# Kernel optimization log

Hardware: AMD Instinct MI355X
Metric: run time of the kernel (lower is better)

The kernel has to match this reference:

```python
import jax, jax.numpy as jnp
import numpy as np

N_U = 100000   # num users
N_V = 50000    # num items
K = 5          # num_support (rating levels)
E_SUP = 400000 # edges per support
E = 500000     # decoder prediction edges
D_IN = 512     # input_dim
D_GCN = 500    # gcn_hidden_dim (D_GCN % K == 0)
D_SIDE = 128   # side_feat_dim
H_SIDE = 64    # side_hidden_dim
D_ENC = 128    # encode_hidden_dim
NB = 3         # num_basis
NC = 5         # num_classes


def setup_inputs() -> dict:
    key = jax.random.key(0)
    ks = jax.random.split(key, 20)
    s = 0.05
    return {
        # sparse supports (COO): user_supports[i] = (N_U,N_V), item_supports[i] = transpose
        "sup_user_idx": jax.random.randint(ks[0], (K, E_SUP), 0, N_U),
        "sup_item_idx": jax.random.randint(ks[1], (K, E_SUP), 0, N_V),
        "sup_vals": jax.random.uniform(ks[2], (K, E_SUP), dtype=jnp.float32),
        "user_inputs": jax.random.normal(ks[3], (N_U, D_IN), dtype=jnp.float32),
        "item_inputs": jax.random.normal(ks[4], (N_V, D_IN), dtype=jnp.float32),
        "user_side_inputs": jax.random.normal(ks[5], (N_U, D_SIDE), dtype=jnp.float32),
        "item_side_inputs": jax.random.normal(ks[6], (N_V, D_SIDE), dtype=jnp.float32),
        "user_edge_idx": jax.random.randint(ks[7], (E,), 0, N_U),
        "item_edge_idx": jax.random.randint(ks[8], (E,), 0, N_V),
        # parameters
        "W_enc": jax.random.normal(ks[9], (K, D_IN, D_GCN // K), dtype=jnp.float32) * s,
        "Wu1": jax.random.normal(ks[10], (D_SIDE, H_SIDE), dtype=jnp.float32) * s,
        "bu1": jnp.zeros((H_SIDE,), dtype=jnp.float32),
        "Wi1": jax.random.normal(ks[11], (D_SIDE, H_SIDE), dtype=jnp.float32) * s,
        "bi1": jnp.zeros((H_SIDE,), dtype=jnp.float32),
        "Wu2": jax.random.normal(ks[12], (D_GCN + H_SIDE, D_ENC), dtype=jnp.float32) * s,
        "Wi2": jax.random.normal(ks[13], (D_GCN + H_SIDE, D_ENC), dtype=jnp.float32) * s,
        "dec_W": jax.random.normal(ks[14], (NB, D_ENC, D_ENC), dtype=jnp.float32) * s,
        "dec_cls": jax.random.normal(ks[15], (NB, NC), dtype=jnp.float32) * s,
    }


def _forward(sup_user_idx, sup_item_idx, sup_vals, user_inputs, item_inputs,
             user_side_inputs, item_side_inputs, user_edge_idx, item_edge_idx,
             W_enc, Wu1, bu1, Wi1, bi1, Wu2, Wi2, dec_W, dec_cls):
    # ---- StackGCNEncoder ----
    tmp_u = jnp.einsum("nd,kdf->knf", user_inputs, W_enc)  # [K, N_U, D_GCN//K]
    tmp_v = jnp.einsum("nd,kdf->knf", item_inputs, W_enc)  # [K, N_V, D_GCN//K]

    def agg_user(rows, cols, vals, xv):  # sparse.mm(user_support, tmp_v)
        return jax.ops.segment_sum(vals[:, None] * xv[cols], rows, num_segments=N_U)

    def agg_item(rows, cols, vals, xu):  # sparse.mm(item_support, tmp_u)
        return jax.ops.segment_sum(vals[:, None] * xu[rows], cols, num_segments=N_V)

    user_hidden = jax.vmap(agg_user)(sup_user_idx, sup_item_idx, sup_vals, tmp_v)  # [K,N_U,f]
    item_hidden = jax.vmap(agg_item)(sup_user_idx, sup_item_idx, sup_vals, tmp_u)  # [K,N_V,f]
    # concat over supports along feature dim
    user_gcn = jax.nn.relu(jnp.transpose(user_hidden, (1, 0, 2)).reshape(N_U, D_GCN))
    item_gcn = jax.nn.relu(jnp.transpose(item_hidden, (1, 0, 2)).reshape(N_V, D_GCN))

    # ---- dense1 (relu, bias) ----
    user_side = jax.nn.relu(user_side_inputs @ Wu1 + bu1)
    item_side = jax.nn.relu(item_side_inputs @ Wi1 + bi1)

    # ---- concat + dense2 (identity activation, no bias) ----
    user_embed = jnp.concatenate([user_gcn, user_side], axis=1) @ Wu2  # [N_U, D_ENC]
    item_embed = jnp.concatenate([item_gcn, item_side], axis=1) @ Wi2  # [N_V, D_ENC]

    # ---- Decoder (bilinear basis, identity activation) ----
    u = user_embed[user_edge_idx]  # [E, D_ENC]
    v = item_embed[item_edge_idx]  # [E, D_ENC]
    basis = jnp.stack([jnp.sum((u @ dec_W[b]) * v, axis=1) for b in range(NB)], axis=1)  # [E, NB]
    return basis @ dec_cls  # [E, NC]


def reference(sup_user_idx, sup_item_idx, sup_vals, user_inputs, item_inputs,
              user_side_inputs, item_side_inputs, user_edge_idx, item_edge_idx,
              W_enc, Wu1, bu1, Wi1, bi1, Wu2, Wi2, dec_W, dec_cls):
    return _forward(sup_user_idx, sup_item_idx, sup_vals, user_inputs, item_inputs,
                    user_side_inputs, item_side_inputs, user_edge_idx, item_edge_idx,
                    W_enc, Wu1, bu1, Wi1, bi1, Wu2, Wi2, dec_W, dec_cls)
```

## Files before the change

### kernel.cpp

```cpp
#include <hip/hip_runtime.h>

#define NU 100000
#define NV 50000
#define KSUP 5
#define ESUP 400000
#define NEDGE (KSUP * ESUP)
#define NE 500000
#define DIN 512
#define DGCN 500
#define FSUP 100
#define DSIDE 128
#define HSIDE 64
#define DENC 128
#define NBAS 3
#define NCLS 5

#define TMPW 640
#define XW 576

#define BNODE 512
#define RU 196
#define RV 98
#define NBU (KSUP * RU)
#define NBV (KSUP * RV)
#define NBT (NBU + NBV)
#define CAPU 2560
#define CAPV 5120
#define CHUNK 8192

#define GU128 782
#define GV128 391
#define GU64 1563
#define GV64 782
#define GBIN 245
#define PB1 (GBIN + 1280)
#define PB2 (PB1 + 288)
#define PB3 (PB2 + 288)
#define PB4 (PB3 + 48)
#define PTOT (PB4 + 75000)

__device__ __forceinline__ ushort f2bf(float x) {
    union { float f; unsigned u; } c; c.f = x;
    unsigned r = (c.u + 0x7FFFu + ((c.u >> 16) & 1u)) >> 16;
    return (ushort)r;
}
__device__ __forceinline__ float lof(uint g) { return __uint_as_float(g << 16); }
__device__ __forceinline__ float hif(uint g) { return __uint_as_float(g & 0xffff0000u); }

typedef __attribute__((ext_vector_type(4))) float f32x4;
typedef __attribute__((ext_vector_type(8))) short bf16x8;
typedef __attribute__((address_space(3))) void lds_void;
typedef const __attribute__((address_space(1))) void glob_void;
typedef unsigned long long ull;

__device__ __forceinline__ void gemm_body(
    const ushort* __restrict__ A, const ushort* __restrict__ BT,
    ushort* __restrict__ Cout, int M, int N, int K, int ldc,
    int rowBase, int colBase)
{
    __shared__ ushort As[128 * 64];
    __shared__ ushort Bs[128 * 64];
    const int t = threadIdx.x;
    const int lane = t & 63;
    const int w = t >> 6;
    const int wr = w >> 1, wc = w & 1;

    f32x4 acc[4][4] = {};

    for (int k0 = 0; k0 < K; k0 += 64) {
        #pragma unroll
        for (int i = 0; i < 4; ++i) {
            int chi = i * 256 + t;
            int r = chi >> 3;
            int c = (((chi >> 3) & 7) ^ (chi & 7)) * 8;
            int ga = rowBase + r; if (ga > M - 1) ga = M - 1;
            __builtin_amdgcn_global_load_lds(
                (glob_void*)(A + (size_t)ga * K + k0 + c),
                (lds_void*)(As + (size_t)chi * 8), 16, 0, 0);
            int gb = colBase + r; if (gb > N - 1) gb = N - 1;
            __builtin_amdgcn_global_load_lds(
                (glob_void*)(BT + (size_t)gb * K + k0 + c),
                (lds_void*)(Bs + (size_t)chi * 8), 16, 0, 0);
        }
        __syncthreads();

        #pragma unroll
        for (int kk = 0; kk < 2; ++kk) {
            bf16x8 af[4], bfr[4];
            const int cb2 = (kk * 32 + (lane >> 4) * 8) * 2;
            #pragma unroll
            for (int mi = 0; mi < 4; ++mi) {
                int r = wr * 64 + mi * 16 + (lane & 15);
                int off = (r * 128 + cb2) ^ ((r & 7) << 4);
                af[mi] = *(const bf16x8*)((const char*)As + off);
            }
            #pragma unroll
            for (int nj = 0; nj < 4; ++nj) {
                int r = wc * 64 + nj * 16 + (lane & 15);
                int off = (r * 128 + cb2) ^ ((r & 7) << 4);
                bfr[nj] = *(const bf16x8*)((const char*)Bs + off);
            }
            #pragma unroll
            for (int mi = 0; mi < 4; ++mi)
                #pragma unroll
                for (int nj = 0; nj < 4; ++nj)
                    acc[mi][nj] = __builtin_amdgcn_mfma_f32_16x16x32_bf16(
                        af[mi], bfr[nj], acc[mi][nj], 0, 0, 0);
        }
        __syncthreads();
    }

    #pragma unroll
    for (int mi = 0; mi < 4; ++mi) {
        #pragma unroll
        for (int q = 0; q < 4; ++q) {
            int gr = rowBase + wr * 64 + mi * 16 + (lane >> 4) * 4 + q;
            if (gr >= M) continue;
            #pragma unroll
            for (int nj = 0; nj < 4; ++nj) {
                int gc = colBase + wc * 64 + nj * 16 + (lane & 15);
                Cout[(size_t)gr * ldc + gc] = f2bf(acc[mi][nj][q]);
            }
        }
    }
}

__global__ __launch_bounds__(256) void gemm_bf16_k(
    const ushort* __restrict__ A, const ushort* __restrict__ BT,
    ushort* __restrict__ Cout, int M, int N, int K, int ldc)
{
    gemm_body(A, BT, Cout, M, N, K, ldc, blockIdx.y * 128, blockIdx.x * 128);
}

__global__ __launch_bounds__(256) void gemm_enc_k(
    const ushort* __restrict__ u_bf, const ushort* __restrict__ v_bf,
    const ushort* __restrict__ WencT2,
    ushort* __restrict__ tmpU, ushort* __restrict__ tmpV)
{
    int y = blockIdx.y;
    const ushort* A; ushort* C; int M, rowBase;
    if (y < GU128) { A = u_bf; C = tmpU; M = NU; rowBase = y * 128; }
    else           { A = v_bf; C = tmpV; M = NV; rowBase = (y - GU128) * 128; }
    gemm_body(A, WencT2, C, M, TMPW, 512, TMPW, rowBase, blockIdx.x * 128);
}

__global__ __launch_bounds__(256) void gemm_d2_k(
    const ushort* __restrict__ Xu, const ushort* __restrict__ Xv,
    const ushort* __restrict__ W2u, const ushort* __restrict__ W2i,
    ushort* __restrict__ embU, ushort* __restrict__ embV)
{
    int y = blockIdx.y;
    const ushort* A; const ushort* BT; ushort* C; int M, rowBase;
    if (y < GU128) { A = Xu; BT = W2u; C = embU; M = NU; rowBase = y * 128; }
    else           { A = Xv; BT = W2i; C = embV; M = NV; rowBase = (y - GU128) * 128; }
    gemm_body(A, BT, C, M, DENC, XW, DENC, rowBase, 0);
}

#define BM 64
#define BK 16
__global__ __launch_bounds__(256) void side_k(
    const float* __restrict__ uS, const float* __restrict__ vS,
    const float* __restrict__ Wu1, const float* __restrict__ bu1,
    const float* __restrict__ Wi1, const float* __restrict__ bi1,
    ushort* __restrict__ Xu, ushort* __restrict__ Xv)
{
    __shared__ float As[BK][BM + 4];
    __shared__ float Bs[BK][BM + 4];
    int b = blockIdx.x;
    const float *A, *B, *bias; ushort* X; int M, rowBase;
    if (b < GU64) { A = uS; B = Wu1; bias = bu1; X = Xu; M = NU; rowBase = b * 64; }
    else          { A = vS; B = Wi1; bias = bi1; X = Xv; M = NV; rowBase = (b - GU64) * 64; }
    const int K = DSIDE;
    const int t = threadIdx.x;
    const int ty = t >> 4, tx = t & 15;
    float acc[4][4] = {};

    for (int k0 = 0; k0 < K; k0 += BK) {
        #pragma unroll
        for (int p = 0; p < 4; ++p) {
            int r = p * 16 + (t >> 4), kk = t & 15;
            int gr = rowBase + r, gk = k0 + kk;
            As[kk][r] = (gr < M && gk < K) ? A[(size_t)gr * K + gk] : 0.f;
        }
        #pragma unroll
        for (int p = 0; p < 4; ++p) {
            int kk = p * 4 + (t >> 6), j = t & 63;
            int gk = k0 + kk;
            Bs[kk][j] = (j < HSIDE && gk < K) ? B[(size_t)gk * HSIDE + j] : 0.f;
        }
        __syncthreads();
        #pragma unroll
        for (int kk = 0; kk < BK; ++kk) {
            float4 a4 = *reinterpret_cast<const float4*>(&As[kk][ty * 4]);
            float4 b4 = *reinterpret_cast<const float4*>(&Bs[kk][tx * 4]);
            float aa[4] = {a4.x, a4.y, a4.z, a4.w};
            float bb[4] = {b4.x, b4.y, b4.z, b4.w};
            #pragma unroll
            for (int i = 0; i < 4; ++i)
                #pragma unroll
                for (int j = 0; j < 4; ++j)
                    acc[i][j] = fmaf(aa[i], bb[j], acc[i][j]);
        }
        __syncthreads();
    }
    #pragma unroll
    for (int i = 0; i < 4; ++i) {
        int gr = rowBase + ty * 4 + i;
        if (gr >= M) continue;
        #pragma unroll
        for (int j = 0; j < 4; ++j) {
            int gc = tx * 4 + j;
            if (gc < HSIDE)
                X[(size_t)gr * XW + 500 + gc] = f2bf(fmaxf(acc[i][j] + bias[gc], 0.f));
        }
    }
}

__global__ __launch_bounds__(256) void prep_k(
    const int* __restrict__ su, const int* __restrict__ si,
    const float* __restrict__ sv,
    int* __restrict__ bCnt, ull* __restrict__ bktU, ull* __restrict__ bktV,
    const float* __restrict__ W_enc, ushort* __restrict__ WencT2,
    const float* __restrict__ Wu2, const float* __restrict__ Wi2,
    ushort* __restrict__ W2ufT, ushort* __restrict__ W2ifT,
    const float* __restrict__ dec_W, ushort* __restrict__ decbf,
    const float* __restrict__ u_in, const float* __restrict__ v_in,
    ushort* __restrict__ u_bf, ushort* __restrict__ v_bf)
{
    __shared__ int lcnt[NBT];
    __shared__ int lbase[NBT];
    const int bid = blockIdx.x;
    const int t = threadIdx.x;

    if (bid < GBIN) {
        const int e0 = bid * CHUNK;
        for (int i = t; i < NBT; i += 256) lcnt[i] = 0;
        __syncthreads();
        for (int i = t; i < CHUNK; i += 256) {
            int e = e0 + i;
            if (e >= NEDGE) break;
            int k = e / ESUP;
            int r = su[e], c = si[e];
            atomicAdd(&lcnt[k * RU + (r >> 9)], 1);
            atomicAdd(&lcnt[NBU + k * RV + (c >> 9)], 1);
        }
        __syncthreads();
        for (int i = t; i < NBT; i += 256) {
            int n = lcnt[i];
            lbase[i] = n ? atomicAdd(&bCnt[i], n) : 0;
        }
        __syncthreads();
        for (int i = t; i < NBT; i += 256) lcnt[i] = 0;
        __syncthreads();
        for (int i = t; i < CHUNK; i += 256) {
            int e = e0 + i;
            if (e >= NEDGE) break;
            int k = e / ESUP;
            int r = su[e], c = si[e];
            ull vb = (ull)(unsigned)__float_as_int(sv[e]) << 32;
            int bu = k * RU + (r >> 9);
            int pu = lbase[bu] + atomicAdd(&lcnt[bu], 1);
            if (pu < CAPU)
                bktU[(size_t)bu * CAPU + pu] = vb | (uint)(((r & 511) << 16) | c);
            int bv = NBU + k * RV + (c >> 9);
            int pv = lbase[bv] + atomicAdd(&lcnt[bv], 1);
            if (pv < CAPV)
                bktV[(size_t)(bv - NBU) * CAPV + pv] = vb | (uint)(((c & 511) << 17) | r);
        }
    } else if (bid < PB1) {
        int idx = (bid - GBIN) * 256 + t;
        int np = idx >> 9, d = idx & 511;
        int k = np >> 7, f = np & 127;
        float v = (f < FSUP) ? W_enc[((size_t)k * DIN + d) * FSUP + f] : 0.f;
        WencT2[idx] = f2bf(v);
    } else if (bid < PB3) {
        int which = (bid < PB2) ? 0 : 1;
        int idx = (bid - (which ? PB2 : PB1)) * 256 + t;
        const float* W = which ? Wi2 : Wu2;
        ushort* out = which ? W2ifT : W2ufT;
        int j = idx / XW, c = idx - j * XW;
        float v = (c < DGCN + HSIDE) ? W[(size_t)c * DENC + j] : 0.f;
        out[idx] = f2bf(v);
    } else if (bid < PB4) {
        long i = ((long)(bid - PB3) * 256 + t) * 4;
        if (i < (long)NBAS * DENC * DENC) {
            float4 v = *(const float4*)(dec_W + i);
            ushort4 o;
            o.x = f2bf(v.x); o.y = f2bf(v.y); o.z = f2bf(v.z); o.w = f2bf(v.w);
            *(ushort4*)(decbf + i) = o;
        }
    } else {
        long i = ((long)(bid - PB4) * 256 + t) * 4;
        const long nu = (long)NU * 512;
        const float* src; ushort* dst;
        if (i < nu) { src = u_in; dst = u_bf; }
        else {
            i -= nu;
            if (i >= (long)NV * 512) return;
            src = v_in; dst = v_bf;
        }
        float4 v = *(const float4*)(src + i);
        ushort4 o;
        o.x = f2bf(v.x); o.y = f2bf(v.y); o.z = f2bf(v.z); o.w = f2bf(v.w);
        *(ushort4*)(dst + i) = o;
    }
}

__global__ __launch_bounds__(256) void scat3_k(
    const int* __restrict__ bCnt,
    const ull* __restrict__ bktU, const ull* __restrict__ bktV,
    int* __restrict__ rowPtrU, int* __restrict__ rowPtrV,
    ull* __restrict__ eU, ull* __restrict__ eV)
{
    __shared__ ull stage[CAPV];
    __shared__ int cnt[BNODE];
    __shared__ int rowOff[BNODE];
    __shared__ int part[256];
    __shared__ int bbl[NBT];
    const int t = threadIdx.x;
    const int b = blockIdx.x;
    const int isU = (b < NBU);

    {
        const int PER = (NBT + 255) / 256;
        int loc[6]; int ssum = 0;
        #pragma unroll
        for (int i = 0; i < PER; ++i) {
            int idx = t * PER + i;
            loc[i] = (idx < NBT) ? bCnt[idx] : 0;
            ssum += loc[i];
        }
        part[t] = ssum; __syncthreads();
        for (int off = 1; off < 256; off <<= 1) {
            int add = (t >= off) ? part[t - off] : 0;
            __syncthreads();
            part[t] += add;
            __syncthreads();
        }
        int bb = part[t] - ssum;
        int run = 0;
        #pragma unroll
        for (int i = 0; i < PER; ++i) {
            int idx = t * PER + i;
            if (idx < NBT) bbl[idx] = bb + run;
            run += loc[i];
        }
        __syncthreads();
    }
    if (b == 0 && t == 0) {
        rowPtrU[KSUP * NU] = NEDGE;
        rowPtrV[KSUP * NV] = NEDGE;
    }

    const ull* src;
    int n, k, baseN, base, NN;
    int* rp;
    if (isU) {
        k = b / RU; baseN = (b % RU) << 9;
        src = bktU + (size_t)b * CAPU;
        n = bCnt[b]; if (n > CAPU) n = CAPU;
        base = bbl[b]; NN = NU; rp = rowPtrU;
    } else {
        int bb2 = b - NBU;
        k = bb2 / RV; baseN = (bb2 % RV) << 9;
        src = bktV + (size_t)bb2 * CAPV;
        n = bCnt[b]; if (n > CAPV) n = CAPV;
        base = bbl[b] - NEDGE; NN = NV; rp = rowPtrV;
    }

    for (int i = t; i < BNODE; i += 256) cnt[i] = 0;
    __syncthreads();

    for (int i = t; i < n; i += 256) {
        ull en = __builtin_nontemporal_load(&src[i]);
        uint w0 = (uint)en;
        int local = isU ? (int)(w0 >> 16) : (int)(w0 >> 17);
        atomicAdd(&cnt[local], 1);
    }
    __syncthreads();

    int c0 = cnt[2 * t], c1 = cnt[2 * t + 1];
    int s = c0 + c1;
    part[t] = s;
    __syncthreads();
    for (int off = 1; off < 256; off <<= 1) {
        int add = (t >= off) ? part[t - off] : 0;
        __syncthreads();
        part[t] += add;
        __syncthreads();
    }
    int excl = part[t] - s;
    cnt[2 * t] = excl;          rowOff[2 * t] = excl;
    cnt[2 * t + 1] = excl + c0; rowOff[2 * t + 1] = excl + c0;
    __syncthreads();

    for (int i = t; i < BNODE; i += 256) {
        int node = baseN + i;
        if (node < NN) rp[k * NN + node] = base + rowOff[i];
    }

    for (int i = t; i < n; i += 256) {
        ull en = __builtin_nontemporal_load(&src[i]);
        uint w0 = (uint)en;
        int local; uint off4;
        if (isU) { local = (int)(w0 >> 16); off4 = (w0 & 0xFFFF) * (TMPW * 2); }
        else     { local = (int)(w0 >> 17); off4 = (w0 & 0x1FFFF) * (TMPW * 2); }
        int p = atomicAdd(&cnt[local], 1);
        stage[p] = (en & 0xFFFFFFFF00000000ull) | off4;
    }
    __syncthreads();

    ull* dst = (isU ? eU : eV) + base;
    for (int i = t; i < n; i += 256)
        __builtin_nontemporal_store(stage[i], &dst[i]);
}

template<int K0, int NK, int B, int NNODE>
__device__ __forceinline__ void agg_do(
    const int* __restrict__ rowPtr, const ull* __restrict__ eArr,
    const char* __restrict__ tSrc, int n, uint lane4,
    float* __restrict__ a0, float* __restrict__ a1)
{
    int s[NK], d[NK];
    #pragma unroll
    for (int kk = 0; kk < NK; ++kk) {
        int g = (K0 + kk) * NNODE + n;
        int ss = rowPtr[g];
        int ee = rowPtr[g + 1];
        s[kk] = ss; d[kk] = ee - ss;
    }
    uint ex[NK][B], ev[NK][B], gw[NK][B];
    #pragma unroll
    for (int kk = 0; kk < NK; ++kk)
        #pragma unroll
        for (int i = 0; i < B; ++i) {
            int idx = (i < d[kk]) ? i : 0;
            ull t = __builtin_nontemporal_load(&eArr[s[kk] + idx]);
            ex[kk][i] = (i < d[kk]) ? (uint)t : 0u;
            ev[kk][i] = (uint)(t >> 32);
        }
    #pragma unroll
    for (int kk = 0; kk < NK; ++kk)
        #pragma unroll
        for (int i = 0; i < B; ++i)
            gw[kk][i] = *(const uint*)(tSrc + (ex[kk][i] + lane4 + ((uint)(K0 + kk) << 8)));
    #pragma unroll
    for (int kk = 0; kk < NK; ++kk) {
        float x0 = 0.f, x1 = 0.f;
        #pragma unroll
        for (int i = 0; i < B; ++i)
            if (i < d[kk]) {
                float v = __uint_as_float(ev[kk][i]);
                x0 = fmaf(v, lof(gw[kk][i]), x0);
                x1 = fmaf(v, hif(gw[kk][i]), x1);
            }
        a0[K0 + kk] = x0; a1[K0 + kk] = x1;
    }
    #pragma unroll
    for (int kk = 0; kk < NK; ++kk) {
        if (d[kk] > B) {
            uint fx[B], fv[B], g1[B];
            #pragma unroll
            for (int i = 0; i < B; ++i) {
                int idx = (B + i < d[kk]) ? B + i : B;
                ull t = __builtin_nontemporal_load(&eArr[s[kk] + idx]);
                fx[i] = (B + i < d[kk]) ? (uint)t : 0u;
                fv[i] = (uint)(t >> 32);
            }
            #pragma unroll
            for (int i = 0; i < B; ++i)
                g1[i] = *(const uint*)(tSrc + (fx[i] + lane4 + ((uint)(K0 + kk) << 8)));
            #pragma unroll
            for (int i = 0; i < B; ++i)
                if (B + i < d[kk]) {
                    float v = __uint_as_float(fv[i]);
                    a0[K0 + kk] = fmaf(v, lof(g1[i]), a0[K0 + kk]);
                    a1[K0 + kk] = fmaf(v, hif(g1[i]), a1[K0 + kk]);
                }
            for (int p = 2 * B; p < d[kk]; ++p) {
                ull t = __builtin_nontemporal_load(&eArr[s[kk] + p]);
                uint g = *(const uint*)(tSrc + ((uint)t + lane4 + ((uint)(K0 + kk) << 8)));
                float v = __uint_as_float((uint)(t >> 32));
                a0[K0 + kk] = fmaf(v, lof(g), a0[K0 + kk]);
                a1[K0 + kk] = fmaf(v, hif(g), a1[K0 + kk]);
            }
        }
    }
}

__device__ __forceinline__ void agg_store(ushort* Xrow, int lane,
                                          const float* a0, const float* a1) {
    #pragma unroll
    for (int k = 0; k < KSUP; ++k) {
        uint payload = (uint)f2bf(fmaxf(a0[k], 0.f)) |
                       ((uint)f2bf(fmaxf(a1[k], 0.f)) << 16);
        if (lane < 50)
            __builtin_nontemporal_store(payload, (uint*)(Xrow + k * FSUP) + lane);
    }
    if (lane < 6)
        __builtin_nontemporal_store(0u, (uint*)(Xrow + 564) + lane);
}

__global__ __launch_bounds__(256) void agg_u_k(
    const int* __restrict__ rowPtrU, const ull* __restrict__ eU,
    const ushort* __restrict__ tmpV, ushort* __restrict__ Xu)
{
    const int lane = threadIdx.x & 63;
    const int n = blockIdx.x * 4 + (threadIdx.x >> 6);
    const uint lane4 = (uint)(((lane < 50) ? lane : 49) << 2);
    float a0[KSUP], a1[KSUP];
    agg_do<0, KSUP, 4, NU>(rowPtrU, eU, (const char*)tmpV, n, lane4, a0, a1);
    agg_store(Xu + (size_t)n * XW, lane, a0, a1);
}

__global__ __launch_bounds__(256) void agg_v_k(
    const int* __restrict__ rowPtrV, const ull* __restrict__ eV,
    const ushort* __restrict__ tmpU, ushort* __restrict__ Xv)
{
    const int lane = threadIdx.x & 63;
    const int n = blockIdx.x * 4 + (threadIdx.x >> 6);
    const uint lane4 = (uint)(((lane < 50) ? lane : 49) << 2);
    float a0[KSUP], a1[KSUP];
    agg_do<0, 3, 8, NV>(rowPtrV, eV, (const char*)tmpU, n, lane4, a0, a1);
    agg_do<3, 2, 8, NV>(rowPtrV, eV, (const char*)tmpU, n, lane4, a0, a1);
    agg_store(Xv + (size_t)n * XW, lane, a0, a1);
}

__global__ __launch_bounds__(256) void dec_k(
    const int* __restrict__ ue, const int* __restrict__ ie,
    const ushort* __restrict__ embU, const ushort* __restrict__ Vb,
    const float* __restrict__ cls, float* __restrict__ out, int nE)
{
    int e = blockIdx.x * 8 + (threadIdx.x >> 5);
    if (e >= nE) return;
    int lane = threadIdx.x & 31;
    int u = ue[e], v = ie[e];
    const int2* pu2 = (const int2*)(embU + (size_t)u * DENC);
    const int2* pv2 = (const int2*)(Vb + (size_t)v * (NBAS * DENC));
    int2 uu = pu2[lane];
    int2 bb[NBAS];
    #pragma unroll
    for (int b = 0; b < NBAS; ++b) bb[b] = pv2[b * 32 + lane];
    float uxl = lof((uint)uu.x), uxh = hif((uint)uu.x);
    float uyl = lof((uint)uu.y), uyh = hif((uint)uu.y);
    float s[NBAS];
    #pragma unroll
    for (int b = 0; b < NBAS; ++b) {
        float t = lof((uint)bb[b].x) * uxl;
        t = fmaf(hif((uint)bb[b].x), uxh, t);
        t = fmaf(lof((uint)bb[b].y), uyl, t);
        s[b] = fmaf(hif((uint)bb[b].y), uyh, t);
    }
    #pragma unroll
    for (int off = 16; off; off >>= 1)
        #pragma unroll
        for (int b = 0; b < NBAS; ++b) s[b] += __shfl_xor(s[b], off, 32);
    if (lane < NCLS) {
        float o = 0.f;
        #pragma unroll
        for (int b = 0; b < NBAS; ++b) o += s[b] * cls[b * NCLS + lane];
        out[(size_t)e * NCLS + lane] = o;
    }
}

extern "C" void kernel_launch(void* const* d_in, const int* in_sizes, int n_in,
                              void* d_out, int out_size, void* d_ws, size_t ws_size,
                              hipStream_t stream) {
    const int*   sup_u  = (const int*)  d_in[0];
    const int*   sup_i  = (const int*)  d_in[1];
    const float* sup_v  = (const float*)d_in[2];
    const float* u_in   = (const float*)d_in[3];
    const float* v_in   = (const float*)d_in[4];
    const float* u_side = (const float*)d_in[5];
    const float* v_side = (const float*)d_in[6];
    const int*   ue     = (const int*)  d_in[7];
    const int*   ie     = (const int*)  d_in[8];
    const float* W_enc  = (const float*)d_in[9];
    const float* Wu1    = (const float*)d_in[10];
    const float* bu1    = (const float*)d_in[11];
    const float* Wi1    = (const float*)d_in[12];
    const float* bi1    = (const float*)d_in[13];
    const float* Wu2    = (const float*)d_in[14];
    const float* Wi2    = (const float*)d_in[15];
    const float* dec_W  = (const float*)d_in[16];
    const float* deccls = (const float*)d_in[17];

    char* ws = (char*)d_ws;
    ushort* u_bf   = (ushort*)(ws);
    ushort* v_bf   = (ushort*)(ws + 102400000LL);
    ushort* Xu     = (ushort*)(ws);
    ushort* Xv     = (ushort*)(ws + 115200000LL);
    int*    rowPtrU= (int*)(ws + 179000000LL);
    int*    rowPtrV= (int*)(ws + 181200000LL);
    int*    bCnt   = (int*)(ws + 185810000LL);
    ull*    eU     = (ull*)(ws + 186000000LL);
    ull*    eV     = (ull*)(ws + 202000000LL);
    ushort* tmpU   = (ushort*)(ws + 220000000LL);
    ushort* tmpV   = (ushort*)(ws + 348000000LL);
    ull*    bktU   = (ull*)(ws + 220000000LL);
    ull*    bktV   = (ull*)(ws + 241000000LL);
    ushort* embUbf = (ushort*)(ws + 176000000LL);
    ushort* embVbf = (ushort*)(ws + 202000000LL);
    ushort* Vb     = (ushort*)(ws + 220000000LL);
    ushort* WencT2 = (ushort*)(ws + 412000000LL);
    ushort* W2ufT  = (ushort*)(ws + 413000000LL);
    ushort* W2ifT  = (ushort*)(ws + 413200000LL);
    ushort* decbf  = (ushort*)(ws + 413400000LL);

    dim3 blk(256);

    hipMemsetAsync(bCnt, 0, 8192, stream);
    prep_k<<<dim3(PTOT), blk, 0, stream>>>(
        sup_u, sup_i, sup_v, bCnt, bktU, bktV,
        W_enc, WencT2, Wu2, Wi2, W2ufT, W2ifT, dec_W, decbf,
        u_in, v_in, u_bf, v_bf);
    scat3_k<<<dim3(NBT), blk, 0, stream>>>(bCnt, bktU, bktV,
                                           rowPtrU, rowPtrV, eU, eV);

    gemm_enc_k<<<dim3(TMPW / 128, GU128 + GV128), blk, 0, stream>>>(
        u_bf, v_bf, WencT2, tmpU, tmpV);

    agg_u_k<<<dim3(NU / 4), blk, 0, stream>>>(rowPtrU, eU, tmpV, Xu);
    agg_v_k<<<dim3(NV / 4), blk, 0, stream>>>(rowPtrV, eV, tmpU, Xv);

    side_k<<<dim3(GU64 + GV64), blk, 0, stream>>>(
        u_side, v_side, Wu1, bu1, Wi1, bi1, Xu, Xv);

    gemm_d2_k<<<dim3(1, GU128 + GV128), blk, 0, stream>>>(
        Xu, Xv, W2ufT, W2ifT, embUbf, embVbf);

    gemm_bf16_k<<<dim3(3, GV128), blk, 0, stream>>>(embVbf, decbf, Vb, NV, 384, 128, 384);

    dec_k<<<dim3(NE / 8), blk, 0, stream>>>(ue, ie, embUbf, Vb, deccls, (float*)d_out, NE);
}
```

Before: 867.9 us.

## Move side MLP into prep kernel, merge aggregation kernels, read side features in dense2

The side-feature dense layer now runs inside the prep kernel and writes to its own bf16 buffers, so it no longer has a separate launch. The user and item aggregation kernels are merged into one launch. The dense2 GEMM gets a custom body that reads the first 512 K-columns from X and the final 64 from the side buffer, which lets X shrink from 576 to 512 columns and the weight layout be remapped to match. This cuts launches and X write traffic, but the prep kernel gets heavier and uses more shared memory.

```diff
diff --git a/kernel.cpp b/kernel.cpp
--- a/kernel.cpp
+++ b/kernel.cpp
@@ -16,7 +16,8 @@
 #define NCLS 5
 
 #define TMPW 640
-#define XW 576
+#define XW 512
+#define KD2 576
 
 #define BNODE 512
 #define RU 196
@@ -32,8 +33,10 @@
 #define GV128 391
 #define GU64 1563
 #define GV64 782
+#define GS (GU64 + GV64)
 #define GBIN 245
-#define PB1 (GBIN + 1280)
+#define PBS (GBIN + GS)
+#define PB1 (PBS + 1280)
 #define PB2 (PB1 + 288)
 #define PB3 (PB2 + 288)
 #define PB4 (PB3 + 48)
@@ -146,76 +149,86 @@
 
 __global__ __launch_bounds__(256) void gemm_d2_k(
     const ushort* __restrict__ Xu, const ushort* __restrict__ Xv,
+    const ushort* __restrict__ sideU, const ushort* __restrict__ sideV,
     const ushort* __restrict__ W2u, const ushort* __restrict__ W2i,
     ushort* __restrict__ embU, ushort* __restrict__ embV)
 {
+    __shared__ ushort As[128 * 64];
+    __shared__ ushort Bs[128 * 64];
     int y = blockIdx.y;
-    const ushort* A; const ushort* BT; ushort* C; int M, rowBase;
-    if (y < GU128) { A = Xu; BT = W2u; C = embU; M = NU; rowBase = y * 128; }
-    else           { A = Xv; BT = W2i; C = embV; M = NV; rowBase = (y - GU128) * 128; }
-    gemm_body(A, BT, C, M, DENC, XW, DENC, rowBase, 0);
-}
-
-#define BM 64
-#define BK 16
-__global__ __launch_bounds__(256) void side_k(
-    const float* __restrict__ uS, const float* __restrict__ vS,
-    const float* __restrict__ Wu1, const float* __restrict__ bu1,
-    const float* __restrict__ Wi1, const float* __restrict__ bi1,
-    ushort* __restrict__ Xu, ushort* __restrict__ Xv)
-{
-    __shared__ float As[BK][BM + 4];
-    __shared__ float Bs[BK][BM + 4];
-    int b = blockIdx.x;
-    const float *A, *B, *bias; ushort* X; int M, rowBase;
-    if (b < GU64) { A = uS; B = Wu1; bias = bu1; X = Xu; M = NU; rowBase = b * 64; }
-    else          { A = vS; B = Wi1; bias = bi1; X = Xv; M = NV; rowBase = (b - GU64) * 64; }
-    const int K = DSIDE;
+    const ushort *X, *S, *BT; ushort* C; int M, rowBase;
+    if (y < GU128) { X = Xu; S = sideU; BT = W2u; C = embU; M = NU; rowBase = y * 128; }
+    else { X = Xv; S = sideV; BT = W2i; C = embV; M = NV; rowBase = (y - GU128) * 128; }
+
     const int t = threadIdx.x;
-    const int ty = t >> 4, tx = t & 15;
-    float acc[4][4] = {};
-
-    for (int k0 = 0; k0 < K; k0 += BK) {
-        #pragma unroll
-        for (int p = 0; p < 4; ++p) {
-            int r = p * 16 + (t >> 4), kk = t & 15;
-            int gr = rowBase + r, gk = k0 + kk;
-            As[kk][r] = (gr < M && gk < K) ? A[(size_t)gr * K + gk] : 0.f;
-        }
-        #pragma unroll
-        for (int p = 0; p < 4; ++p) {
-            int kk = p * 4 + (t >> 6), j = t & 63;
-            int gk = k0 + kk;
-            Bs[kk][j] = (j < HSIDE && gk < K) ? B[(size_t)gk * HSIDE + j] : 0.f;
-        }
-        __syncthreads();
-        #pragma unroll
-        for (int kk = 0; kk < BK; ++kk) {
-            float4 a4 = *reinterpret_cast<const float4*>(&As[kk][ty * 4]);
-            float4 b4 = *reinterpret_cast<const float4*>(&Bs[kk][tx * 4]);
-            float aa[4] = {a4.x, a4.y, a4.z, a4.w};
-            float bb[4] = {b4.x, b4.y, b4.z, b4.w};
-            #pragma unroll
-            for (int i = 0; i < 4; ++i)
+    const int lane = t & 63;
+    const int w = t >> 6;
+    const int wr = w >> 1, wc = w & 1;
+
+    f32x4 acc[4][4] = {};
+
+    for (int k0 = 0; k0 < KD2; k0 += 64) {
+        const bool fromX = (k0 < XW);
+        #pragma unroll
+        for (int i = 0; i < 4; ++i) {
+            int chi = i * 256 + t;
+            int r = chi >> 3;
+            int c = (((chi >> 3) & 7) ^ (chi & 7)) * 8;
+            int ga = rowBase + r; if (ga > M - 1) ga = M - 1;
+            const ushort* src = fromX ? (X + (size_t)ga * XW + k0 + c)
+                                      : (S + (size_t)ga * HSIDE + c);
+            __builtin_amdgcn_global_load_lds(
+                (glob_void*)src, (lds_void*)(As + (size_t)chi * 8), 16, 0, 0);
+            int gb = r;
+            __builtin_amdgcn_global_load_lds(
+                (glob_void*)(BT + (size_t)gb * KD2 + k0 + c),
+                (lds_void*)(Bs + (size_t)chi * 8), 16, 0, 0);
+        }
+        __syncthreads();
+
+        #pragma unroll
+        for (int kk = 0; kk < 2; ++kk) {
+            bf16x8 af[4], bfr[4];
+            const int cb2 = (kk * 32 + (lane >> 4) * 8) * 2;
+            #pragma unroll
+            for (int mi = 0; mi < 4; ++mi) {
+                int r = wr * 64 + mi * 16 + (lane & 15);
+                int off = (r * 128 + cb2) ^ ((r & 7) << 4);
+                af[mi] = *(const bf16x8*)((const char*)As + off);
+            }
+            #pragma unroll
+            for (int nj = 0; nj < 4; ++nj) {
+                int r = wc * 64 + nj * 16 + (lane & 15);
+                int off = (r * 128 + cb2) ^ ((r & 7) << 4);
+                bfr[nj] = *(const bf16x8*)((const char*)Bs + off);
+            }
+            #pragma unroll
+            for (int mi = 0; mi < 4; ++mi)
                 #pragma unroll
-                for (int j = 0; j < 4; ++j)
-                    acc[i][j] = fmaf(aa[i], bb[j], acc[i][j]);
-        }
-        __syncthreads();
-    }
-    #pragma unroll
-    for (int i = 0; i < 4; ++i) {
-        int gr = rowBase + ty * 4 + i;
-        if (gr >= M) continue;
-        #pragma unroll
-        for (int j = 0; j < 4; ++j) {
-            int gc = tx * 4 + j;
-            if (gc < HSIDE)
-                X[(size_t)gr * XW + 500 + gc] = f2bf(fmaxf(acc[i][j] + bias[gc], 0.f));
-        }
-    }
-}
-
+                for (int nj = 0; nj < 4; ++nj)
+                    acc[mi][nj] = __builtin_amdgcn_mfma_f32_16x16x32_bf16(
+                        af[mi], bfr[nj], acc[mi][nj], 0, 0, 0);
+        }
+        __syncthreads();
+    }
+
+    #pragma unroll
+    for (int mi = 0; mi < 4; ++mi) {
+        #pragma unroll
+        for (int q = 0; q < 4; ++q) {
+            int gr = rowBase + wr * 64 + mi * 16 + (lane >> 4) * 4 + q;
+            if (gr >= M) continue;
+            #pragma unroll
+            for (int nj = 0; nj < 4; ++nj) {
+                int gc = wc * 64 + nj * 16 + (lane & 15);
+                C[(size_t)gr * DENC + gc] = f2bf(acc[mi][nj][q]);
+            }
+        }
+    }
+}
+
+#define SBM 64
+#define SBK 16
 __global__ __launch_bounds__(256) void prep_k(
     const int* __restrict__ su, const int* __restrict__ si,
     const float* __restrict__ sv,
@@ -225,14 +238,19 @@
     ushort* __restrict__ W2ufT, ushort* __restrict__ W2ifT,
     const float* __restrict__ dec_W, ushort* __restrict__ decbf,
     const float* __restrict__ u_in, const float* __restrict__ v_in,
-    ushort* __restrict__ u_bf, ushort* __restrict__ v_bf)
-{
-    __shared__ int lcnt[NBT];
-    __shared__ int lbase[NBT];
+    ushort* __restrict__ u_bf, ushort* __restrict__ v_bf,
+    const float* __restrict__ uS, const float* __restrict__ vS,
+    const float* __restrict__ Wu1, const float* __restrict__ bu1,
+    const float* __restrict__ Wi1, const float* __restrict__ bi1,
+    ushort* __restrict__ sideU, ushort* __restrict__ sideV)
+{
+    __shared__ __align__(16) char smem[2 * NBT * 4];
     const int bid = blockIdx.x;
     const int t = threadIdx.x;
 
     if (bid < GBIN) {
+        int* lcnt  = (int*)smem;
+        int* lbase = (int*)(smem + NBT * 4);
         const int e0 = bid * CHUNK;
         for (int i = t; i < NBT; i += 256) lcnt[i] = 0;
         __syncthreads();
@@ -267,8 +285,54 @@
             if (pv < CAPV)
                 bktV[(size_t)(bv - NBU) * CAPV + pv] = vb | (uint)(((c & 511) << 17) | r);
         }
+    } else if (bid < PBS) {
+        float (*As)[SBM + 4] = (float (*)[SBM + 4])smem;
+        float (*Bs)[SBM + 4] = (float (*)[SBM + 4])(smem + SBK * (SBM + 4) * 4);
+        int b = bid - GBIN;
+        const float *A, *B, *bias; ushort* O; int M, rowBase;
+        if (b < GU64) { A = uS; B = Wu1; bias = bu1; O = sideU; M = NU; rowBase = b * 64; }
+        else { A = vS; B = Wi1; bias = bi1; O = sideV; M = NV; rowBase = (b - GU64) * 64; }
+        const int ty = t >> 4, tx = t & 15;
+        float acc[4][4] = {};
+        for (int k0 = 0; k0 < DSIDE; k0 += SBK) {
+            #pragma unroll
+            for (int p = 0; p < 4; ++p) {
+                int r = p * 16 + (t >> 4), kk = t & 15;
+                int gr = rowBase + r, gk = k0 + kk;
+                As[kk][r] = (gr < M) ? A[(size_t)gr * DSIDE + gk] : 0.f;
+            }
+            #pragma unroll
+            for (int p = 0; p < 4; ++p) {
+                int kk = p * 4 + (t >> 6), j = t & 63;
+                Bs[kk][j] = B[(size_t)(k0 + kk) * HSIDE + j];
+            }
+            __syncthreads();
+            #pragma unroll
+            for (int kk = 0; kk < SBK; ++kk) {
+                float4 a4 = *reinterpret_cast<const float4*>(&As[kk][ty * 4]);
+                float4 b4 = *reinterpret_cast<const float4*>(&Bs[kk][tx * 4]);
+                float aa[4] = {a4.x, a4.y, a4.z, a4.w};
+                float bb[4] = {b4.x, b4.y, b4.z, b4.w};
+                #pragma unroll
+                for (int i = 0; i < 4; ++i)
+                    #pragma unroll
+                    for (int j = 0; j < 4; ++j)
+                        acc[i][j] = fmaf(aa[i], bb[j], acc[i][j]);
+            }
+            __syncthreads();
+        }
+        #pragma unroll
+        for (int i = 0; i < 4; ++i) {
+            int gr = rowBase + ty * 4 + i;
+            if (gr >= M) continue;
+            #pragma unroll
+            for (int j = 0; j < 4; ++j) {
+                int gc = tx * 4 + j;
+                O[(size_t)gr * HSIDE + gc] = f2bf(fmaxf(acc[i][j] + bias[gc], 0.f));
+            }
+        }
     } else if (bid < PB1) {
-        int idx = (bid - GBIN) * 256 + t;
+        int idx = (bid - PBS) * 256 + t;
         int np = idx >> 9, d = idx & 511;
         int k = np >> 7, f = np & 127;
         float v = (f < FSUP) ? W_enc[((size_t)k * DIN + d) * FSUP + f] : 0.f;
@@ -278,8 +342,10 @@
         int idx = (bid - (which ? PB2 : PB1)) * 256 + t;
         const float* W = which ? Wi2 : Wu2;
         ushort* out = which ? W2ifT : W2ufT;
-        int j = idx / XW, c = idx - j * XW;
-        float v = (c < DGCN + HSIDE) ? W[(size_t)c * DENC + j] : 0.f;
+        int j = idx / KD2, c = idx - j * KD2;
+        float v = 0.f;
+        if (c < DGCN) v = W[(size_t)c * DENC + j];
+        else if (c >= XW) v = W[(size_t)(c - 12) * DENC + j];
         out[idx] = f2bf(v);
     } else if (bid < PB4) {
         long i = ((long)(bid - PB3) * 256 + t) * 4;
@@ -498,32 +564,29 @@
             __builtin_nontemporal_store(payload, (uint*)(Xrow + k * FSUP) + lane);
     }
     if (lane < 6)
-        __builtin_nontemporal_store(0u, (uint*)(Xrow + 564) + lane);
-}
-
-__global__ __launch_bounds__(256) void agg_u_k(
+        __builtin_nontemporal_store(0u, (uint*)(Xrow + 500) + lane);
+}
+
+__global__ __launch_bounds__(256) void agg_k(
     const int* __restrict__ rowPtrU, const ull* __restrict__ eU,
-    const ushort* __restrict__ tmpV, ushort* __restrict__ Xu)
+    const int* __restrict__ rowPtrV, const ull* __restrict__ eV,
+    const ushort* __restrict__ tmpU, const ushort* __restrict__ tmpV,
+    ushort* __restrict__ Xu, ushort* __restrict__ Xv)
 {
     const int lane = threadIdx.x & 63;
-    const int n = blockIdx.x * 4 + (threadIdx.x >> 6);
     const uint lane4 = (uint)(((lane < 50) ? lane : 49) << 2);
+    const int b = blockIdx.x;
     float a0[KSUP], a1[KSUP];
-    agg_do<0, KSUP, 4, NU>(rowPtrU, eU, (const char*)tmpV, n, lane4, a0, a1);
-    agg_store(Xu + (size_t)n * XW, lane, a0, a1);
-}
-
-__global__ __launch_bounds__(256) void agg_v_k(
-    const int* __restrict__ rowPtrV, const ull* __restrict__ eV,
-    const ushort* __restrict__ tmpU, ushort* __restrict__ Xv)
-{
-    const int lane = threadIdx.x & 63;
-    const int n = blockIdx.x * 4 + (threadIdx.x >> 6);
-    const uint lane4 = (uint)(((lane < 50) ? lane : 49) << 2);
-    float a0[KSUP], a1[KSUP];
-    agg_do<0, 3, 8, NV>(rowPtrV, eV, (const char*)tmpU, n, lane4, a0, a1);
-    agg_do<3, 2, 8, NV>(rowPtrV, eV, (const char*)tmpU, n, lane4, a0, a1);
-    agg_store(Xv + (size_t)n * XW, lane, a0, a1);
+    if (b < NU / 4) {
+        const int n = b * 4 + (threadIdx.x >> 6);
+        agg_do<0, KSUP, 4, NU>(rowPtrU, eU, (const char*)tmpV, n, lane4, a0, a1);
+        agg_store(Xu + (size_t)n * XW, lane, a0, a1);
+    } else {
+        const int n = (b - NU / 4) * 4 + (threadIdx.x >> 6);
+        agg_do<0, 3, 8, NV>(rowPtrV, eV, (const char*)tmpU, n, lane4, a0, a1);
+        agg_do<3, 2, 8, NV>(rowPtrV, eV, (const char*)tmpU, n, lane4, a0, a1);
+        agg_store(Xv + (size_t)n * XW, lane, a0, a1);
+    }
 }
 
 __global__ __launch_bounds__(256) void dec_k(
@@ -589,7 +652,7 @@
     ushort* u_bf   = (ushort*)(ws);
     ushort* v_bf   = (ushort*)(ws + 102400000LL);
     ushort* Xu     = (ushort*)(ws);
-    ushort* Xv     = (ushort*)(ws + 115200000LL);
+    ushort* Xv     = (ushort*)(ws + 102400000LL);
     int*    rowPtrU= (int*)(ws + 179000000LL);
     int*    rowPtrV= (int*)(ws + 181200000LL);
     int*    bCnt   = (int*)(ws + 185810000LL);
@@ -606,6 +669,8 @@
     ushort* W2ufT  = (ushort*)(ws + 413000000LL);
     ushort* W2ifT  = (ushort*)(ws + 413200000LL);
     ushort* decbf  = (ushort*)(ws + 413400000LL);
+    ushort* sideU  = (ushort*)(ws + 413600000LL);
+    ushort* sideV  = (ushort*)(ws + 426400000LL);
 
     dim3 blk(256);
 
@@ -613,21 +678,19 @@
     prep_k<<<dim3(PTOT), blk, 0, stream>>>(
         sup_u, sup_i, sup_v, bCnt, bktU, bktV,
         W_enc, WencT2, Wu2, Wi2, W2ufT, W2ifT, dec_W, decbf,
-        u_in, v_in, u_bf, v_bf);
+        u_in, v_in, u_bf, v_bf,
+        u_side, v_side, Wu1, bu1, Wi1, bi1, sideU, sideV);
     scat3_k<<<dim3(NBT), blk, 0, stream>>>(bCnt, bktU, bktV,
                                            rowPtrU, rowPtrV, eU, eV);
 
     gemm_enc_k<<<dim3(TMPW / 128, GU128 + GV128), blk, 0, stream>>>(
         u_bf, v_bf, WencT2, tmpU, tmpV);
 
-    agg_u_k<<<dim3(NU / 4), blk, 0, stream>>>(rowPtrU, eU, tmpV, Xu);
-    agg_v_k<<<dim3(NV / 4), blk, 0, stream>>>(rowPtrV, eV, tmpU, Xv);
-
-    side_k<<<dim3(GU64 + GV64), blk, 0, stream>>>(
-        u_side, v_side, Wu1, bu1, Wi1, bi1, Xu, Xv);
+    agg_k<<<dim3(NU / 4 + NV / 4), blk, 0, stream>>>(
+        rowPtrU, eU, rowPtrV, eV, tmpU, tmpV, Xu, Xv);
 
     gemm_d2_k<<<dim3(1, GU128 + GV128), blk, 0, stream>>>(
-        Xu, Xv, W2ufT, W2ifT, embUbf, embVbf);
+        Xu, Xv, sideU, sideV, W2ufT, W2ifT, embUbf, embVbf);
 
     gemm_bf16_k<<<dim3(3, GV128), blk, 0, stream>>>(embVbf, decbf, Vb, NV, 384, 128, 384);
 
```

Result: faster. 839.8 us (-3.2%).
